# Optimization experiments

Measured on AMD Instinct MI355X. Metric: run time of the kernel, lower is better.

The kernel has to match this reference:

```python
import jax, jax.numpy as jnp
import numpy as np

N, LQ, D_MODEL, M_HEADS, P_POINTS, H_DIM, W_DIM = 8, 4096, 256, 8, 4, 64, 64


def setup_inputs() -> dict:
    key = jax.random.key(0)
    ks = jax.random.split(key, 9)
    d = D_MODEL
    scale = 1.0 / np.sqrt(d).astype(np.float32)
    return {
        "query": jax.random.normal(ks[0], (N, LQ, d), jnp.float32),
        "reference_points": jax.random.uniform(ks[1], (N, LQ, 2), jnp.float32),
        "input_flatten": jax.random.normal(ks[2], (N, H_DIM * W_DIM, d), jnp.float32),
        "H": H_DIM,
        "W": W_DIM,
        "Wv": jax.random.normal(ks[3], (d, d), jnp.float32) * scale,
        "bv": jnp.zeros((d,), jnp.float32),
        "Woff": jax.random.normal(ks[4], (M_HEADS * P_POINTS * 2, d), jnp.float32) * 0.01,
        "boff": jax.random.normal(ks[5], (M_HEADS * P_POINTS * 2,), jnp.float32) * 0.5,
        "Wa": jax.random.normal(ks[6], (M_HEADS * P_POINTS, d), jnp.float32) * 0.01,
        "ba": jnp.zeros((M_HEADS * P_POINTS,), jnp.float32),
        "Wo": jax.random.normal(ks[7], (d, d), jnp.float32) * scale,
        "bo": jnp.zeros((d,), jnp.float32),
    }


def _bilinear_sample(val, grid, H, W):
    # val: [B, D, H*W]; grid: [B, Lq, P, 2] in [-1, 1] (x, y); align_corners=False, zero padding.
    B, D, _ = val.shape
    _, Lq, P, _ = grid.shape
    x = (grid[..., 0] + 1.0) * (W * 0.5) - 0.5
    y = (grid[..., 1] + 1.0) * (H * 0.5) - 0.5
    x0 = jnp.floor(x)
    y0 = jnp.floor(y)
    x0i = x0.astype(jnp.int32)
    y0i = y0.astype(jnp.int32)
    wx1 = x - x0
    wy1 = y - y0
    out = jnp.zeros((B, D, Lq, P), val.dtype)
    for xi, wx in ((x0i, 1.0 - wx1), (x0i + 1, wx1)):
        for yi, wy in ((y0i, 1.0 - wy1), (y0i + 1, wy1)):
            valid = (xi >= 0) & (xi < W) & (yi >= 0) & (yi < H)
            idx = jnp.clip(yi, 0, H - 1) * W + jnp.clip(xi, 0, W - 1)  # [B, Lq, P]
            g = jnp.take_along_axis(val, idx.reshape(B, 1, Lq * P), axis=2).reshape(B, D, Lq, P)
            w = jnp.where(valid, wx * wy, 0.0)
            out = out + g * w[:, None]
    return out


def reference(query, reference_points, input_flatten, H, W, Wv, bv, Woff, boff, Wa, ba, Wo, bo):
    n, lq, d = query.shape
    m, p = M_HEADS, P_POINTS
    dh = d // m
    value = (input_flatten @ Wv.T + bv).reshape(n, H * W, m, dh)
    offsets = (query @ Woff.T + boff).reshape(n, lq, m, p, 2)
    attw = jax.nn.softmax((query @ Wa.T + ba).reshape(n, lq, m, p), axis=-1)
    normalizer = jnp.array([W, H], dtype=query.dtype)  # [W, H] order per torch code
    loc = reference_points[:, :, None, None, :] + offsets / normalizer
    grid = 2.0 * loc - 1.0  # [n, lq, m, p, 2]
    # value -> [n*m, dh, H*W] matching torch flatten(2).transpose(1,2).reshape
    val = jnp.transpose(value, (0, 2, 3, 1)).reshape(n * m, dh, H * W)
    grd = jnp.transpose(grid, (0, 2, 1, 3, 4)).reshape(n * m, lq, p, 2)
    samp = _bilinear_sample(val, grd, H, W)  # [n*m, dh, lq, p]
    aw = jnp.transpose(attw, (0, 2, 1, 3)).reshape(n * m, 1, lq, p)
    out = (samp * aw).sum(-1).reshape(n, m * dh, lq)
    out = jnp.transpose(out, (0, 2, 1))  # [n, lq, d]
    return out @ Wo.T + bo
```

## Files before the change

### kernel.cpp

```cpp
#include <hip/hip_runtime.h>
#include <math.h>

#define NB   8
#define LQN  4096
#define DM   256
#define MH   8
#define PP   4
#define HH   64
#define WW   64
#define LG   128
#define PW   67
#define PPIX (PW*PW)

typedef __bf16 bf16x8 __attribute__((ext_vector_type(8)));
typedef float  f32x4  __attribute__((ext_vector_type(4)));
typedef unsigned short us8 __attribute__((ext_vector_type(8)));
typedef unsigned short us4 __attribute__((ext_vector_type(4)));

__device__ __forceinline__ unsigned short f2bf(float f) {
    unsigned u = __float_as_uint(f);
    u += 0x7FFFu + ((u >> 16) & 1u);
    return (unsigned short)(u >> 16);
}
__device__ __forceinline__ float bf2f(unsigned short b) {
    return __uint_as_float((unsigned)b << 16);
}

__device__ __forceinline__ void gl2lds16(const void* g, unsigned short* l) {
    __builtin_amdgcn_global_load_lds(
        (const __attribute__((address_space(1))) void*)g,
        (__attribute__((address_space(3))) void*)l,
        16, 0, 0);
}

__device__ __forceinline__ bf16x8 cvt_frag(const unsigned short* s, int row, int kq) {
    const int u0 = row * 8 + ((kq * 2) ^ (row & 7));
    const int u1 = u0 ^ 1;
    const f32x4 a0 = *(const f32x4*)&s[u0 * 8];
    const f32x4 a1 = *(const f32x4*)&s[u1 * 8];
    bf16x8 v;
    v[0] = (__bf16)a0[0]; v[1] = (__bf16)a0[1];
    v[2] = (__bf16)a0[2]; v[3] = (__bf16)a0[3];
    v[4] = (__bf16)a1[0]; v[5] = (__bf16)a1[1];
    v[6] = (__bf16)a1[2]; v[7] = (__bf16)a1[3];
    return v;
}

__global__ __launch_bounds__(256)
void prep_kernel(const float* __restrict__ Wv, const float* __restrict__ Wo,
                 const float* __restrict__ Woff, const float* __restrict__ Wa,
                 const float* __restrict__ boff, const float* __restrict__ ba,
                 unsigned short* __restrict__ Wvh, unsigned short* __restrict__ Woh,
                 unsigned short* __restrict__ Wcath, float* __restrict__ bcat,
                 unsigned short* __restrict__ valueP) {
    const int i = blockIdx.x * 256 + threadIdx.x;
    if (i < 65536) {
        Wvh[i] = f2bf(Wv[i]);
    } else if (i < 131072) {
        const int j = i - 65536;
        Woh[j] = f2bf(Wo[j]);
    } else if (i < 163840) {
        const int j = i - 131072, n = j >> 8, k = j & 255;
        const float v = (n < 64) ? Woff[n * 256 + k]
                                 : ((n < 96) ? Wa[(n - 64) * 256 + k] : 0.f);
        Wcath[j] = f2bf(v);
    } else if (i < 163968) {
        const int n = i - 163840;
        bcat[n] = (n < 64) ? boff[n] : ((n < 96) ? ba[n - 64] : 0.f);
    } else if (i < 163968 + 201216) {
        const int j   = i - 163968;
        const int c4  = j & 63;
        const int pix = j >> 6;
        const int n   = pix / 393;
        const int r   = pix - n * 393;
        int x, y;
        if (r < 201) {
            const int q = r / 67;
            y = (q == 0) ? 0 : (q == 1 ? 65 : 66);
            x = r - q * 67;
        } else {
            const int q = r - 201;
            y = 1 + q / 3;
            const int s = q - (q / 3) * 3;
            x = (s == 0) ? 0 : (s == 1 ? 65 : 66);
        }
        const size_t addr = ((size_t)n * PPIX + (size_t)y * PW + x) * DM + c4 * 4;
        *(ushort4*)&valueP[addr] = make_ushort4(0, 0, 0, 0);
    }
}

__global__ __launch_bounds__(256, 4)
void dual_gemm(const float* __restrict__ Ain, const float* __restrict__ Aq,
               const unsigned short* __restrict__ Wvh,
               const unsigned short* __restrict__ Wcath,
               const float* __restrict__ bv, const float* __restrict__ bcat,
               unsigned short* __restrict__ valueP,
               unsigned short* __restrict__ logitsB) {
    constexpr int K = 256, NK = 8;
    __shared__ unsigned short sA[2][4096];
    __shared__ unsigned short sB[2][4096];

    const int t   = threadIdx.x;
    const int blk = blockIdx.x;
    const bool isVal = (blk < 1024);

    const float* A; const unsigned short* B; const float* bias;
    int brow, bcol;
    if (isVal) {
        const int x   = blk & 7;
        const int idx = blk >> 3;
        brow = x * 4096 + (idx >> 1) * 64;
        bcol = (idx & 1) * 128;
        A = Ain; B = Wvh; bias = bv;
    } else {
        const int blk2 = blk - 1024;
        brow = (blk2 & 7) * 4096 + (blk2 >> 3) * 64;
        bcol = 0;
        A = Aq; B = Wcath; bias = bcat;
    }

    const int srow = t >> 3;
    const int scq  = (t & 7) ^ (srow & 7);
    const float* aG = A + (size_t)(brow + srow) * K + scq * 4;
    const size_t aI = (size_t)32 * K;

    const unsigned short* bG = B + (size_t)(bcol + (t >> 2)) * K + (t & 3) * 8;
    const size_t bI = (size_t)64 * K;

    const int l   = t & 63;
    const int wid = t >> 6;
    const int wr  = wid >> 1, wc = wid & 1;
    const int fr  = l & 15,   kq = l >> 4;

    f32x4 acc[2][4] = {};

#define STAGE(buf, ks_) { const int k0_ = (ks_) * 32;                    \
       gl2lds16(aG + k0_,      &sA[buf][t * 8]);                         \
       gl2lds16(aG + k0_ + aI, &sA[buf][2048 + t * 8]);                  \
       gl2lds16(bG + k0_,      &sB[buf][t * 8]);                         \
       gl2lds16(bG + k0_ + bI, &sB[buf][2048 + t * 8]); }

    STAGE(0, 0);
    STAGE(1, 1);

    for (int ks = 0; ks < NK; ++ks) {
        const int cur = ks & 1;
        if (ks < NK - 1) asm volatile("s_waitcnt vmcnt(4)" ::: "memory");
        else             asm volatile("s_waitcnt vmcnt(0)" ::: "memory");
        __builtin_amdgcn_s_barrier();
        __builtin_amdgcn_sched_barrier(0);

        bf16x8 af[2], bf_[4];
#pragma unroll
        for (int m = 0; m < 2; ++m)
            af[m]  = cvt_frag(sA[cur], wr * 32 + m * 16 + fr, kq);
#pragma unroll
        for (int n = 0; n < 4; ++n)
            bf_[n] = *(const bf16x8*)&sB[cur][(wc * 64 + n * 16 + fr) * 32 + kq * 8];

#pragma unroll
        for (int m = 0; m < 2; ++m)
#pragma unroll
            for (int n = 0; n < 4; ++n)
                acc[m][n] = __builtin_amdgcn_mfma_f32_16x16x32_bf16(
                    bf_[n], af[m], acc[m][n], 0, 0, 0);

        __builtin_amdgcn_sched_barrier(0);
        __builtin_amdgcn_s_barrier();
        if (ks + 2 < NK) STAGE(cur, ks + 2);
    }
#undef STAGE

#pragma unroll
    for (int m = 0; m < 2; ++m) {
        const int row = brow + wr * 32 + m * 16 + fr;
        size_t rbase;
        if (isVal) {
            const int nb_ = row >> 12;
            const int pix = row & 4095;
            const int y   = pix >> 6, x = pix & 63;
            rbase = ((size_t)nb_ * PPIX + (size_t)(y + 1) * PW + (x + 1)) * DM;
        } else {
            rbase = (size_t)row * LG;
        }
#pragma unroll
        for (int n = 0; n < 4; ++n) {
            const int colq = bcol + wc * 64 + n * 16 + kq * 4;
            const float4 b4 = *(const float4*)&bias[colq];
            us4 o;
            o[0] = f2bf(acc[m][n][0] + b4.x);
            o[1] = f2bf(acc[m][n][1] + b4.y);
            o[2] = f2bf(acc[m][n][2] + b4.z);
            o[3] = f2bf(acc[m][n][3] + b4.w);
            *(us4*)&(isVal ? valueP : logitsB)[rbase + colq] = o;
        }
    }
}

__global__ __launch_bounds__(256, 4)
void gemm_out(const unsigned short* __restrict__ A,
              const unsigned short* __restrict__ B,
              const float* __restrict__ bias, float* __restrict__ C) {
    constexpr int K = 256, N = DM, NK = 8;
    __shared__ unsigned short sA[2][4096];
    __shared__ unsigned short sB[2][4096];

    const int t   = threadIdx.x;
    const int blk = blockIdx.x;
    const int x   = blk & 7;
    const int idx = blk >> 3;
    const int brow = x * 4096 + (idx >> 1) * 128;
    const int bcol = (idx & 1) * 128;

    const unsigned short* aG = A + (size_t)(brow + (t >> 2)) * K + (t & 3) * 8;
    const unsigned short* bG = B + (size_t)(bcol + (t >> 2)) * K + (t & 3) * 8;
    const size_t rs64 = (size_t)64 * K;

    const int l   = t & 63;
    const int wid = t >> 6;
    const int wr  = wid >> 1, wc = wid & 1;
    const int fr  = l & 15,   kq = l >> 4;

    f32x4 acc[4][4] = {};

#define STAGEO(buf, ks_) { const int k0_ = (ks_) * 32;                   \
       gl2lds16(aG + k0_,        &sA[buf][t * 8]);                       \
       gl2lds16(aG + k0_ + rs64, &sA[buf][2048 + t * 8]);                \
       gl2lds16(bG + k0_,        &sB[buf][t * 8]);                       \
       gl2lds16(bG + k0_ + rs64, &sB[buf][2048 + t * 8]); }

    STAGEO(0, 0);
    STAGEO(1, 1);

    for (int ks = 0; ks < NK; ++ks) {
        const int cur = ks & 1;
        if (ks < NK - 1) asm volatile("s_waitcnt vmcnt(4)" ::: "memory");
        else             asm volatile("s_waitcnt vmcnt(0)" ::: "memory");
        __builtin_amdgcn_s_barrier();
        __builtin_amdgcn_sched_barrier(0);

        bf16x8 af[4], bfr[4];
#pragma unroll
        for (int m = 0; m < 4; ++m)
            af[m]  = *(const bf16x8*)&sA[cur][(wr * 64 + m * 16 + fr) * 32 + kq * 8];
#pragma unroll
        for (int n = 0; n < 4; ++n)
            bfr[n] = *(const bf16x8*)&sB[cur][(wc * 64 + n * 16 + fr) * 32 + kq * 8];

#pragma unroll
        for (int m = 0; m < 4; ++m)
#pragma unroll
            for (int n = 0; n < 4; ++n)
                acc[m][n] = __builtin_amdgcn_mfma_f32_16x16x32_bf16(
                    bfr[n], af[m], acc[m][n], 0, 0, 0);

        __builtin_amdgcn_sched_barrier(0);
        __builtin_amdgcn_s_barrier();
        if (ks + 2 < NK) STAGEO(cur, ks + 2);
    }
#undef STAGEO

#pragma unroll
    for (int m = 0; m < 4; ++m) {
        const int row = brow + wr * 64 + m * 16 + fr;
#pragma unroll
        for (int n = 0; n < 4; ++n) {
            const int colq = bcol + wc * 64 + n * 16 + kq * 4;
            const float4 bs = *(const float4*)&bias[colq];
            float4 o;
            o.x = acc[m][n][0] + bs.x; o.y = acc[m][n][1] + bs.y;
            o.z = acc[m][n][2] + bs.z; o.w = acc[m][n][3] + bs.w;
            *(float4*)&C[(size_t)row * N + colq] = o;
        }
    }
}

__global__ __launch_bounds__(256)
void sample_kernel(const float* __restrict__ refp,
                   const unsigned short* __restrict__ valueP,
                   const unsigned short* __restrict__ logitsB,
                   unsigned short* __restrict__ sampledH) {
    const int vb   = (blockIdx.x & 7) * 1024 + (blockIdx.x >> 3);
    const int wid  = threadIdx.x >> 6;
    const int b    = vb * 4 + wid;
    const int n    = b >> 12;
    const int lane = threadIdx.x & 63;

    const int tp  = lane & 31;
    const int pm  = tp >> 2, ppt = tp & 3;
    const unsigned short* lg = logitsB + (size_t)b * LG;

    const float rx = refp[(size_t)b * 2 + 0];
    const float ry = refp[(size_t)b * 2 + 1];
    const float ox = bf2f(lg[pm * 8 + ppt * 2 + 0]);
    const float oy = bf2f(lg[pm * 8 + ppt * 2 + 1]);
    const float la = bf2f(lg[64 + tp]);

    const float x = fminf(fmaxf(fmaf(rx, (float)WW, ox) - 0.5f, -1.0f), 64.0f);
    const float y = fminf(fmaxf(fmaf(ry, (float)HH, oy) - 0.5f, -1.0f), 64.0f);

    float mx = fmaxf(la, __shfl_xor(la, 1));
    mx = fmaxf(mx, __shfl_xor(mx, 2));
    const float e = __expf(la - mx);
    float den = e + __shfl_xor(e, 1);
    den += __shfl_xor(den, 2);
    const float w = e / den;

    const int half = lane >> 5;
    const int c8   = lane & 31;
    const int mh   = c8 >> 2;
    const unsigned short* vbase = valueP + (size_t)n * (PPIX * DM) + c8 * 8;

    float accv[8] = {};
#pragma unroll
    for (int p = 0; p < PP; ++p) {
        const int   sl = mh * PP + p;
        const float xp = __shfl(x, sl);
        const float yp = __shfl(y, sl);
        const float wp = __shfl(w, sl);

        const float x0f = floorf(xp), y0f = floorf(yp);
        const int   x0 = (int)x0f,   y0 = (int)y0f;
        const float wx1 = xp - x0f,  wy1 = yp - y0f;
        const float wy  = half ? wy1 : (1.f - wy1);
        const float wA  = wp * wy * (1.f - wx1);
        const float wB  = wp * wy * wx1;

        const unsigned short* p0 =
            vbase + (size_t)((y0 + 1 + half) * PW + (x0 + 1)) * DM;
        const us8 gA = *(const us8*)(p0);
        const us8 gB = *(const us8*)(p0 + DM);
#pragma unroll
        for (int j = 0; j < 8; ++j) {
            accv[j] = fmaf(wA, bf2f(gA[j]), accv[j]);
            accv[j] = fmaf(wB, bf2f(gB[j]), accv[j]);
        }
    }

#pragma unroll
    for (int j = 0; j < 8; ++j)
        accv[j] += __shfl_xor(accv[j], 32);

    if (half == 0) {
        us8 o;
#pragma unroll
        for (int j = 0; j < 8; ++j) o[j] = f2bf(accv[j]);
        *(us8*)&sampledH[(size_t)b * DM + c8 * 8] = o;
    }
}

extern "C" void kernel_launch(void* const* d_in, const int* in_sizes, int n_in,
                              void* d_out, int out_size, void* d_ws, size_t ws_size,
                              hipStream_t stream) {
    const float* query  = (const float*)d_in[0];
    const float* refp   = (const float*)d_in[1];
    const float* inputf = (const float*)d_in[2];
    const float* Wv   = (const float*)d_in[5];
    const float* bv   = (const float*)d_in[6];
    const float* Woff = (const float*)d_in[7];
    const float* boff = (const float*)d_in[8];
    const float* Wa   = (const float*)d_in[9];
    const float* ba   = (const float*)d_in[10];
    const float* Wo   = (const float*)d_in[11];
    const float* bo   = (const float*)d_in[12];
    float* out = (float*)d_out;

    const int Mrows = NB * LQN;

    unsigned short* sampledH = (unsigned short*)d_ws;
    unsigned short* valueP   = sampledH + (size_t)Mrows * DM;
    unsigned short* logitsB  = valueP   + (size_t)NB * PPIX * DM;
    unsigned short* Wvh      = logitsB  + (size_t)Mrows * LG;
    unsigned short* Woh      = Wvh      + 65536;
    unsigned short* Wcath    = Woh      + 65536;
    float*          bcat     = (float*)(Wcath + 32768);

    prep_kernel<<<1427, 256, 0, stream>>>(Wv, Wo, Woff, Wa, boff, ba,
                                          Wvh, Woh, Wcath, bcat, valueP);

    dual_gemm<<<1536, 256, 0, stream>>>(inputf, query, Wvh, Wcath, bv, bcat,
                                        valueP, logitsB);

    sample_kernel<<<Mrows / 4, 256, 0, stream>>>(refp, valueP, logitsB, sampledH);

    gemm_out<<<512, 256, 0, stream>>>(sampledH, Woh, bo, out);
}
```

Before: 62.40 us.

## Fuse bilinear sampling into output GEMM via LDS-resident sampled tile

Merges the sampling kernel and the output projection GEMM into one kernel. Each 512-thread block samples 64 query rows into a swizzled LDS tile (bf16) and then multiplies that tile by the output weight, streamed through double-buffered LDS. This drops the global write and reread of the sampled intermediate and one launch. The cost is 64KB of dynamic LDS per block, which limits occupancy. Sampling also runs serially per wave, 8 rows each, and that latency is no longer hidden by a separate high-occupancy launch.

```diff
diff --git a/kernel.cpp b/kernel.cpp
--- a/kernel.cpp
+++ b/kernel.cpp
@@ -197,58 +197,127 @@
     }
 }
 
-__global__ __launch_bounds__(256, 4)
-void gemm_out(const unsigned short* __restrict__ A,
-              const unsigned short* __restrict__ B,
-              const float* __restrict__ bias, float* __restrict__ C) {
-    constexpr int K = 256, N = DM, NK = 8;
-    __shared__ unsigned short sA[2][4096];
-    __shared__ unsigned short sB[2][4096];
-
-    const int t   = threadIdx.x;
-    const int blk = blockIdx.x;
-    const int x   = blk & 7;
-    const int idx = blk >> 3;
-    const int brow = x * 4096 + (idx >> 1) * 128;
-    const int bcol = (idx & 1) * 128;
-
-    const unsigned short* aG = A + (size_t)(brow + (t >> 2)) * K + (t & 3) * 8;
-    const unsigned short* bG = B + (size_t)(bcol + (t >> 2)) * K + (t & 3) * 8;
-    const size_t rs64 = (size_t)64 * K;
-
-    const int l   = t & 63;
-    const int wid = t >> 6;
-    const int wr  = wid >> 1, wc = wid & 1;
-    const int fr  = l & 15,   kq = l >> 4;
-
-    f32x4 acc[4][4] = {};
-
-#define STAGEO(buf, ks_) { const int k0_ = (ks_) * 32;                   \
-       gl2lds16(aG + k0_,        &sA[buf][t * 8]);                       \
-       gl2lds16(aG + k0_ + rs64, &sA[buf][2048 + t * 8]);                \
-       gl2lds16(bG + k0_,        &sB[buf][t * 8]);                       \
-       gl2lds16(bG + k0_ + rs64, &sB[buf][2048 + t * 8]); }
-
-    STAGEO(0, 0);
-    STAGEO(1, 1);
+__global__ __launch_bounds__(512, 4)
+void fused_sample_out(const float* __restrict__ refp,
+                      const unsigned short* __restrict__ valueP,
+                      const unsigned short* __restrict__ logitsB,
+                      const unsigned short* __restrict__ Woh,
+                      const float* __restrict__ bo, float* __restrict__ C) {
+    constexpr int K = 256, NK = 8;
+    extern __shared__ unsigned short smem[];
+    unsigned short* sS = smem;
+    unsigned short* sB = smem + 16384;
+
+    const int t    = threadIdx.x;
+    const int blk  = blockIdx.x;
+    const int nb   = blk & 7;
+    const int brow = nb * 4096 + (blk >> 3) * 64;
+    const int w    = t >> 6;
+    const int lane = t & 63;
+
+    {
+        const int tp  = lane & 31;
+        const int pm  = tp >> 2, ppt = tp & 3;
+        const int half = lane >> 5;
+        const int c8   = lane & 31;
+        const int mh   = c8 >> 2;
+        const unsigned short* vbase = valueP + (size_t)nb * (PPIX * DM) + c8 * 8;
+
+        for (int i = 0; i < 8; ++i) {
+            const int q = w * 8 + i;
+            const int b = brow + q;
+            const unsigned short* lg = logitsB + (size_t)b * LG;
+
+            const float rx = refp[(size_t)b * 2 + 0];
+            const float ry = refp[(size_t)b * 2 + 1];
+            const float ox = bf2f(lg[pm * 8 + ppt * 2 + 0]);
+            const float oy = bf2f(lg[pm * 8 + ppt * 2 + 1]);
+            const float la = bf2f(lg[64 + tp]);
+
+            const float x = fminf(fmaxf(fmaf(rx, (float)WW, ox) - 0.5f, -1.0f), 64.0f);
+            const float y = fminf(fmaxf(fmaf(ry, (float)HH, oy) - 0.5f, -1.0f), 64.0f);
+
+            float mx = fmaxf(la, __shfl_xor(la, 1));
+            mx = fmaxf(mx, __shfl_xor(mx, 2));
+            const float e = __expf(la - mx);
+            float den = e + __shfl_xor(e, 1);
+            den += __shfl_xor(den, 2);
+            const float wgt = e / den;
+
+            float accv[8] = {};
+#pragma unroll
+            for (int p = 0; p < PP; ++p) {
+                const int   sl = mh * PP + p;
+                const float xp = __shfl(x, sl);
+                const float yp = __shfl(y, sl);
+                const float wp = __shfl(wgt, sl);
+
+                const float x0f = floorf(xp), y0f = floorf(yp);
+                const int   x0 = (int)x0f,   y0 = (int)y0f;
+                const float wx1 = xp - x0f,  wy1 = yp - y0f;
+                const float wy  = half ? wy1 : (1.f - wy1);
+                const float wA  = wp * wy * (1.f - wx1);
+                const float wB  = wp * wy * wx1;
+
+                const unsigned short* p0 =
+                    vbase + (size_t)((y0 + 1 + half) * PW + (x0 + 1)) * DM;
+                const us8 gA = *(const us8*)(p0);
+                const us8 gB = *(const us8*)(p0 + DM);
+#pragma unroll
+                for (int j = 0; j < 8; ++j) {
+                    accv[j] = fmaf(wA, bf2f(gA[j]), accv[j]);
+                    accv[j] = fmaf(wB, bf2f(gB[j]), accv[j]);
+                }
+            }
+#pragma unroll
+            for (int j = 0; j < 8; ++j)
+                accv[j] += __shfl_xor(accv[j], 32);
+
+            if (half == 0) {
+                us8 o;
+#pragma unroll
+                for (int j = 0; j < 8; ++j) o[j] = f2bf(accv[j]);
+                *(us8*)&sS[q * 256 + ((c8 ^ (q & 7)) * 8)] = o;
+            }
+        }
+    }
+    __syncthreads();
+
+    const unsigned short* bG = Woh + (size_t)(t >> 2) * K + (t & 3) * 8;
+    const size_t rHalf = (size_t)128 * K;
+
+    const int wr = w >> 2, wc = w & 3;
+    const int fr = lane & 15, kq = lane >> 4;
+
+    f32x4 acc[2][4] = {};
+
+#define STAGEF(buf, ks_) { const int k0_ = (ks_) * 32;                   \
+       gl2lds16(bG + k0_,         &sB[(buf) * 8192 + t * 8]);            \
+       gl2lds16(bG + k0_ + rHalf, &sB[(buf) * 8192 + 4096 + t * 8]); }
+
+    STAGEF(0, 0);
+    STAGEF(1, 1);
 
     for (int ks = 0; ks < NK; ++ks) {
         const int cur = ks & 1;
-        if (ks < NK - 1) asm volatile("s_waitcnt vmcnt(4)" ::: "memory");
+        if (ks < NK - 1) asm volatile("s_waitcnt vmcnt(2)" ::: "memory");
         else             asm volatile("s_waitcnt vmcnt(0)" ::: "memory");
         __builtin_amdgcn_s_barrier();
         __builtin_amdgcn_sched_barrier(0);
 
-        bf16x8 af[4], bfr[4];
-#pragma unroll
-        for (int m = 0; m < 4; ++m)
-            af[m]  = *(const bf16x8*)&sA[cur][(wr * 64 + m * 16 + fr) * 32 + kq * 8];
+        bf16x8 af[2], bfr[4];
+#pragma unroll
+        for (int m = 0; m < 2; ++m) {
+            const int row = wr * 32 + m * 16 + fr;
+            const int u   = (ks * 4 + kq) ^ (row & 7);
+            af[m] = *(const bf16x8*)&sS[row * 256 + u * 8];
+        }
 #pragma unroll
         for (int n = 0; n < 4; ++n)
-            bfr[n] = *(const bf16x8*)&sB[cur][(wc * 64 + n * 16 + fr) * 32 + kq * 8];
-
-#pragma unroll
-        for (int m = 0; m < 4; ++m)
+            bfr[n] = *(const bf16x8*)&sB[cur * 8192 + (wc * 64 + n * 16 + fr) * 32 + kq * 8];
+
+#pragma unroll
+        for (int m = 0; m < 2; ++m)
 #pragma unroll
             for (int n = 0; n < 4; ++n)
                 acc[m][n] = __builtin_amdgcn_mfma_f32_16x16x32_bf16(
@@ -256,96 +325,22 @@
 
         __builtin_amdgcn_sched_barrier(0);
         __builtin_amdgcn_s_barrier();
-        if (ks + 2 < NK) STAGEO(cur, ks + 2);
-    }
-#undef STAGEO
-
-#pragma unroll
-    for (int m = 0; m < 4; ++m) {
-        const int row = brow + wr * 64 + m * 16 + fr;
+        if (ks + 2 < NK) STAGEF(cur, ks + 2);
+    }
+#undef STAGEF
+
+#pragma unroll
+    for (int m = 0; m < 2; ++m) {
+        const int row = brow + wr * 32 + m * 16 + fr;
 #pragma unroll
         for (int n = 0; n < 4; ++n) {
-            const int colq = bcol + wc * 64 + n * 16 + kq * 4;
-            const float4 bs = *(const float4*)&bias[colq];
+            const int colq = wc * 64 + n * 16 + kq * 4;
+            const float4 bs = *(const float4*)&bo[colq];
             float4 o;
             o.x = acc[m][n][0] + bs.x; o.y = acc[m][n][1] + bs.y;
             o.z = acc[m][n][2] + bs.z; o.w = acc[m][n][3] + bs.w;
-            *(float4*)&C[(size_t)row * N + colq] = o;
-        }
-    }
-}
-
-__global__ __launch_bounds__(256)
-void sample_kernel(const float* __restrict__ refp,
-                   const unsigned short* __restrict__ valueP,
-                   const unsigned short* __restrict__ logitsB,
-                   unsigned short* __restrict__ sampledH) {
-    const int vb   = (blockIdx.x & 7) * 1024 + (blockIdx.x >> 3);
-    const int wid  = threadIdx.x >> 6;
-    const int b    = vb * 4 + wid;
-    const int n    = b >> 12;
-    const int lane = threadIdx.x & 63;
-
-    const int tp  = lane & 31;
-    const int pm  = tp >> 2, ppt = tp & 3;
-    const unsigned short* lg = logitsB + (size_t)b * LG;
-
-    const float rx = refp[(size_t)b * 2 + 0];
-    const float ry = refp[(size_t)b * 2 + 1];
-    const float ox = bf2f(lg[pm * 8 + ppt * 2 + 0]);
-    const float oy = bf2f(lg[pm * 8 + ppt * 2 + 1]);
-    const float la = bf2f(lg[64 + tp]);
-
-    const float x = fminf(fmaxf(fmaf(rx, (float)WW, ox) - 0.5f, -1.0f), 64.0f);
-    const float y = fminf(fmaxf(fmaf(ry, (float)HH, oy) - 0.5f, -1.0f), 64.0f);
-
-    float mx = fmaxf(la, __shfl_xor(la, 1));
-    mx = fmaxf(mx, __shfl_xor(mx, 2));
-    const float e = __expf(la - mx);
-    float den = e + __shfl_xor(e, 1);
-    den += __shfl_xor(den, 2);
-    const float w = e / den;
-
-    const int half = lane >> 5;
-    const int c8   = lane & 31;
-    const int mh   = c8 >> 2;
-    const unsigned short* vbase = valueP + (size_t)n * (PPIX * DM) + c8 * 8;
-
-    float accv[8] = {};
-#pragma unroll
-    for (int p = 0; p < PP; ++p) {
-        const int   sl = mh * PP + p;
-        const float xp = __shfl(x, sl);
-        const float yp = __shfl(y, sl);
-        const float wp = __shfl(w, sl);
-
-        const float x0f = floorf(xp), y0f = floorf(yp);
-        const int   x0 = (int)x0f,   y0 = (int)y0f;
-        const float wx1 = xp - x0f,  wy1 = yp - y0f;
-        const float wy  = half ? wy1 : (1.f - wy1);
-        const float wA  = wp * wy * (1.f - wx1);
-        const float wB  = wp * wy * wx1;
-
-        const unsigned short* p0 =
-            vbase + (size_t)((y0 + 1 + half) * PW + (x0 + 1)) * DM;
-        const us8 gA = *(const us8*)(p0);
-        const us8 gB = *(const us8*)(p0 + DM);
-#pragma unroll
-        for (int j = 0; j < 8; ++j) {
-            accv[j] = fmaf(wA, bf2f(gA[j]), accv[j]);
-            accv[j] = fmaf(wB, bf2f(gB[j]), accv[j]);
-        }
-    }
-
-#pragma unroll
-    for (int j = 0; j < 8; ++j)
-        accv[j] += __shfl_xor(accv[j], 32);
-
-    if (half == 0) {
-        us8 o;
-#pragma unroll
-        for (int j = 0; j < 8; ++j) o[j] = f2bf(accv[j]);
-        *(us8*)&sampledH[(size_t)b * DM + c8 * 8] = o;
+            *(float4*)&C[(size_t)row * DM + colq] = o;
+        }
     }
 }
 
@@ -367,8 +362,7 @@
 
     const int Mrows = NB * LQN;
 
-    unsigned short* sampledH = (unsigned short*)d_ws;
-    unsigned short* valueP   = sampledH + (size_t)Mrows * DM;
+    unsigned short* valueP   = (unsigned short*)d_ws;
     unsigned short* logitsB  = valueP   + (size_t)NB * PPIX * DM;
     unsigned short* Wvh      = logitsB  + (size_t)Mrows * LG;
     unsigned short* Woh      = Wvh      + 65536;
@@ -381,7 +375,6 @@
     dual_gemm<<<1536, 256, 0, stream>>>(inputf, query, Wvh, Wcath, bv, bcat,
                                         valueP, logitsB);
 
-    sample_kernel<<<Mrows / 4, 256, 0, stream>>>(refp, valueP, logitsB, sampledH);
-
-    gemm_out<<<512, 256, 0, stream>>>(sampledH, Woh, bo, out);
-}
+    fused_sample_out<<<512, 512, 65536, stream>>>(refp, valueP, logitsB,
+                                                  Woh, bo, out);
+}
```

Measured after the change: 59.87 us. 4.0% less time.
